# Optimization experiments

Hardware: AMD Instinct MI355X
Metric: run time of the kernel (lower is better)

## Reference

```python
import jax, jax.numpy as jnp
import numpy as np

B, S, D = 2, 2048, 1024
H, HD = 16, 64
SCALE = HD ** -0.5  # applied TWICE (q pre-scale + inference score scale), matching the source


def setup_inputs() -> dict:
    key = jax.random.key(0)
    ks = jax.random.split(key, 6)
    std = 0.02
    return {
        "x": jax.random.normal(ks[0], (B, S, D), dtype=jnp.float32),
        "Wq": jax.random.normal(ks[1], (D, D), dtype=jnp.float32) * std,
        "Wk": jax.random.normal(ks[2], (D, D), dtype=jnp.float32) * std,
        "Wv": jax.random.normal(ks[3], (D, D), dtype=jnp.float32) * std,
        "Wo": jax.random.normal(ks[4], (D, D), dtype=jnp.float32) * std,
        "bo": jnp.zeros((D,), dtype=jnp.float32),
    }


def reference(x, Wq, Wk, Wv, Wo, bo):
    b, s, d = x.shape
    # nn.Linear: y = x @ W^T ; split heads: b s (h hd) -> b h s hd
    def split_heads(y):
        return y.reshape(b, s, H, HD).transpose(0, 2, 1, 3)

    q = split_heads(x @ Wq.T) * SCALE          # forward pre-scales q
    k = split_heads(x @ Wk.T)
    v = split_heads(x @ Wv.T)

    # inference path scales scores by SCALE again (double scaling, faithful)
    scores = jnp.einsum("bhsd,bhtd->bhst", q, k) * SCALE  # [B,H,S,S]
    causal = jnp.triu(jnp.full((s, s), -jnp.inf, dtype=scores.dtype), k=1)
    scores = scores + causal[None, None]

    # explicit stable softmax as in the source
    m = jnp.max(scores, axis=-1, keepdims=True)
    e = jnp.exp(scores - m)
    attn = e / jnp.sum(e, axis=-1, keepdims=True)

    out = jnp.einsum("bhst,bhtd->bhsd", attn, v)          # [B,H,S,HD]
    out = out.transpose(0, 2, 1, 3).reshape(b, s, d)       # b h s hd -> b s (h hd)
    return out @ Wo.T + bo
```

## Files before the change

### kernel.cpp

```cpp
#include <hip/hip_runtime.h>
#include <stdint.h>

#define S_LEN 2048
#define DMODEL 1024
#define NHEAD 16
#define HDIM 64
#define BATCH 2

typedef float f32x4 __attribute__((ext_vector_type(4)));
typedef __bf16 bf16x8 __attribute__((ext_vector_type(8)));

typedef const void __attribute__((address_space(1)))* as1_cvp;
typedef void __attribute__((address_space(3)))* as3_vp;

__device__ __forceinline__ ushort f2bf(float f) {
    union { float f; unsigned u; } v; v.f = f;
    unsigned u = v.u;
    return (ushort)((u + 0x7fffu + ((u >> 16) & 1u)) >> 16);
}

__device__ __forceinline__ void gload16(const void* g, void* l) {
    __builtin_amdgcn_global_load_lds((as1_cvp)g, (as3_vp)l, 16, 0, 0);
}

template<int N> __device__ __forceinline__ void wait_vm_barrier() {
    if constexpr (N == 0)      asm volatile("s_waitcnt vmcnt(0)" ::: "memory");
    else if constexpr (N == 3) asm volatile("s_waitcnt vmcnt(3)" ::: "memory");
    else if constexpr (N == 4) asm volatile("s_waitcnt vmcnt(4)" ::: "memory");
    else                       asm volatile("s_waitcnt vmcnt(0)" ::: "memory");
    asm volatile("s_barrier" ::: "memory");
}

__global__ __launch_bounds__(256) void cvt_all(
    const float* __restrict__ x,  const float* __restrict__ wq,
    const float* __restrict__ wk, const float* __restrict__ wv,
    const float* __restrict__ wo,
    ushort* __restrict__ xb, ushort* __restrict__ wqkv, ushort* __restrict__ wob,
    float qscale) {
    const float* src; ushort* dst; int n; float sc = 1.0f;
    const int DD = DMODEL * DMODEL;
    switch (blockIdx.y) {
        case 0: src = x;  dst = xb;            n = BATCH * S_LEN * DMODEL; break;
        case 1: src = wq; dst = wqkv;          n = DD; sc = qscale; break;
        case 2: src = wk; dst = wqkv + DD;     n = DD; break;
        case 3: src = wv; dst = wqkv + 2 * DD; n = DD; break;
        default: src = wo; dst = wob;          n = DD; break;
    }
    const int step = gridDim.x * 256 * 8;
    for (int i = (blockIdx.x * 256 + threadIdx.x) * 8; i < n; i += step) {
        float4 a = *(const float4*)(src + i);
        float4 b = *(const float4*)(src + i + 4);
        union { ushort us[8]; int4 v; } r;
        r.us[0] = f2bf(a.x * sc); r.us[1] = f2bf(a.y * sc);
        r.us[2] = f2bf(a.z * sc); r.us[3] = f2bf(a.w * sc);
        r.us[4] = f2bf(b.x * sc); r.us[5] = f2bf(b.y * sc);
        r.us[6] = f2bf(b.z * sc); r.us[7] = f2bf(b.w * sc);
        *(int4*)(dst + i) = r.v;
    }
}

template<int BM, int BN, bool F32OUT, bool BIAS>
__global__ __launch_bounds__(256) void gemm_nt(
    const ushort* __restrict__ A, const ushort* __restrict__ B,
    void* __restrict__ Cv, const float* __restrict__ bias,
    int M, int N, int K) {
    __shared__ ushort As0[BM][32], As1[BM][32], As2[BM][32];
    __shared__ ushort Bs0[BN][32], Bs1[BN][32], Bs2[BN][32];
    constexpr int MR = BM / 32, NR = BN / 32, AG = BM / 64, BG = BN / 64;
    constexpr int LPS = AG + BG;
    const int tid = threadIdx.x;
    const int wave = tid >> 6, lane = tid & 63;
    const int wm = (wave >> 1) * (BM / 2), wn = (wave & 1) * (BN / 2);
    const int bm = blockIdx.x * BM, bn = blockIdx.y * BN;
    const int l15 = lane & 15, lg = lane >> 4;
    f32x4 acc[MR][NR] = {};

    const int sr = lane >> 2, scol = (lane & 3) * 8;
    const ushort* gA[AG]; const ushort* gB[BG];
    int rA0[AG], rB0[BG];
#pragma unroll
    for (int i = 0; i < AG; i++) {
        rA0[i] = wave * (BM / 4) + i * 16;
        gA[i] = A + (size_t)(bm + rA0[i] + sr) * K + scol;
    }
#pragma unroll
    for (int i = 0; i < BG; i++) {
        rB0[i] = wave * (BN / 4) + i * 16;
        gB[i] = B + (size_t)(bn + rB0[i] + sr) * K + scol;
    }

    auto STAGE = [&](int t, ushort (*as)[32], ushort (*bs)[32]) {
        const int off = t * 32;
#pragma unroll
        for (int i = 0; i < AG; i++) gload16(gA[i] + off, &as[rA0[i]][0]);
#pragma unroll
        for (int i = 0; i < BG; i++) gload16(gB[i] + off, &bs[rB0[i]][0]);
    };
    auto COMPUTE = [&](ushort (*as)[32], ushort (*bs)[32]) {
        bf16x8 af[MR], bfr[NR];
#pragma unroll
        for (int m = 0; m < MR; m++) {
            int4 t_ = *(const int4*)&as[wm + m * 16 + l15][lg * 8];
            af[m] = __builtin_bit_cast(bf16x8, t_);
        }
#pragma unroll
        for (int n = 0; n < NR; n++) {
            int4 t_ = *(const int4*)&bs[wn + n * 16 + l15][lg * 8];
            bfr[n] = __builtin_bit_cast(bf16x8, t_);
        }
        __builtin_amdgcn_s_setprio(1);
#pragma unroll
        for (int m = 0; m < MR; m++)
#pragma unroll
            for (int n = 0; n < NR; n++)
                acc[m][n] = __builtin_amdgcn_mfma_f32_16x16x32_bf16(af[m], bfr[n], acc[m][n], 0, 0, 0);
        __builtin_amdgcn_s_setprio(0);
    };

    const int NT = K / 32;
    STAGE(0, As0, Bs0);
    STAGE(1, As1, Bs1);
    wait_vm_barrier<LPS>();

    int t = 0;
    for (; t + 5 <= NT; t += 3) {
        STAGE(t + 2, As2, Bs2); COMPUTE(As0, Bs0); wait_vm_barrier<LPS>();
        STAGE(t + 3, As0, Bs0); COMPUTE(As1, Bs1); wait_vm_barrier<LPS>();
        STAGE(t + 4, As1, Bs1); COMPUTE(As2, Bs2); wait_vm_barrier<LPS>();
    }
    COMPUTE(As0, Bs0);
    wait_vm_barrier<0>();
    COMPUTE(As1, Bs1);

    float* Cf = (float*)Cv;
    ushort* Cb = (ushort*)Cv;
#pragma unroll
    for (int m = 0; m < MR; m++) {
        const int row = bm + wm + m * 16 + lg * 4;
#pragma unroll
        for (int n = 0; n < NR; n++) {
            const int col = bn + wn + n * 16 + l15;
            const float bb = BIAS ? bias[col] : 0.0f;
#pragma unroll
            for (int j = 0; j < 4; j++) {
                float v = acc[m][n][j];
                if (F32OUT) Cf[(size_t)(row + j) * N + col] = v + bb;
                else        Cb[(size_t)(row + j) * N + col] = f2bf(v);
            }
        }
    }
}

__global__ __launch_bounds__(256) void attn_fwd(
    const ushort* __restrict__ QKV, ushort* __restrict__ Og) {
    __shared__ ushort Ks[2][64][72];
    __shared__ ushort Vt[2][64][72];
    __shared__ ushort Ps[4][16][76];
    const int tid = threadIdx.x;
    const int wave = tid >> 6, lane = tid & 63;
    const int l15 = lane & 15, lg = lane >> 4;
    const int qt = 31 - (blockIdx.x >> 5);
    const int bh = blockIdx.x & 31;
    const int b = bh >> 4, h = bh & 15;
    const int q0 = qt * 64;
    const ushort* Qb = QKV + (size_t)b * S_LEN * 3072 + h * HDIM;
    const ushort* Kb = Qb + 1024;
    const ushort* Vb = Qb + 2048;

    const int4 onesi = {0x3F803F80, 0x3F803F80, 0x3F803F80, 0x3F803F80};
    const bf16x8 ones = __builtin_bit_cast(bf16x8, onesi);

    bf16x8 qf[2];
#pragma unroll
    for (int kk = 0; kk < 2; kk++) {
        int4 t = *(const int4*)(Qb + (size_t)(q0 + wave * 16 + l15) * 3072 + kk * 32 + lg * 8);
        qf[kk] = __builtin_bit_cast(bf16x8, t);
    }

    f32x4 o[4] = {};
    f32x4 lacc = {};

    const int kr = tid >> 2, kc = (tid & 3) * 8;
    const int vt_ = tid & 63, vh = (tid >> 6) * 8;
    int4 kreg0, kreg1, vreg0, vreg1;

    auto LOAD = [&](int t) {
        const ushort* kp = Kb + (size_t)(t * 64 + kr) * 3072 + kc;
        kreg0 = *(const int4*)kp;
        kreg1 = *(const int4*)(kp + 32);
        const ushort* vp = Vb + (size_t)(t * 64 + vt_) * 3072 + vh;
        vreg0 = *(const int4*)vp;
        vreg1 = *(const int4*)(vp + 32);
    };
    auto STORE = [&](int buf) {
        *(int4*)&Ks[buf][kr][kc]      = kreg0;
        *(int4*)&Ks[buf][kr][kc + 32] = kreg1;
        union { int4 v; ushort us[8]; } u0, u1;
        u0.v = vreg0; u1.v = vreg1;
#pragma unroll
        for (int j = 0; j < 8; j++) Vt[buf][vh + j][vt_] = u0.us[j];
#pragma unroll
        for (int j = 0; j < 8; j++) Vt[buf][32 + vh + j][vt_] = u1.us[j];
    };

    auto COMPUTE = [&](bool diag, int cur) {
        f32x4 s[4] = {};
        __builtin_amdgcn_s_setprio(1);
#pragma unroll
        for (int kk = 0; kk < 2; kk++) {
#pragma unroll
            for (int n = 0; n < 4; n++) {
                int4 t = *(const int4*)&Ks[cur][n * 16 + l15][kk * 32 + lg * 8];
                s[n] = __builtin_amdgcn_mfma_f32_16x16x32_bf16(qf[kk], __builtin_bit_cast(bf16x8, t), s[n], 0, 0, 0);
            }
        }
        __builtin_amdgcn_s_setprio(0);
        if (diag) {
            const int qrow = wave * 16 + lg * 4;
#pragma unroll
            for (int n = 0; n < 4; n++) {
                const int tg = n * 16 + l15;
#pragma unroll
                for (int j = 0; j < 4; j++)
                    if (tg > qrow + j) s[n][j] = -1e30f;
            }
        }
#pragma unroll
        for (int n = 0; n < 4; n++)
#pragma unroll
            for (int j = 0; j < 4; j++)
                Ps[wave][lg * 4 + j][n * 16 + l15] = f2bf(__expf(s[n][j]));
        asm volatile("s_waitcnt lgkmcnt(0)" ::: "memory");
        __builtin_amdgcn_s_setprio(1);
#pragma unroll
        for (int kk = 0; kk < 2; kk++) {
            int4 tp = *(const int4*)&Ps[wave][l15][kk * 32 + lg * 8];
            bf16x8 pf = __builtin_bit_cast(bf16x8, tp);
#pragma unroll
            for (int n = 0; n < 4; n++) {
                int4 tv = *(const int4*)&Vt[cur][n * 16 + l15][kk * 32 + lg * 8];
                o[n] = __builtin_amdgcn_mfma_f32_16x16x32_bf16(pf, __builtin_bit_cast(bf16x8, tv), o[n], 0, 0, 0);
            }
            lacc = __builtin_amdgcn_mfma_f32_16x16x32_bf16(pf, ones, lacc, 0, 0, 0);
        }
        __builtin_amdgcn_s_setprio(0);
    };

    LOAD(0);
    STORE(0);
    __syncthreads();

    for (int t0 = 0; t0 <= qt; ++t0) {
        const int cur = t0 & 1;
        if (t0 < qt) LOAD(t0 + 1);
        COMPUTE(t0 == qt, cur);
        if (t0 < qt) {
            STORE(cur ^ 1);
            __syncthreads();
        }
    }

#pragma unroll
    for (int j = 0; j < 4; j++) lacc[j] = 1.0f / lacc[j];
#pragma unroll
    for (int n = 0; n < 4; n++)
#pragma unroll
        for (int j = 0; j < 4; j++) {
            const int qrow = q0 + wave * 16 + lg * 4 + j;
            Og[((size_t)(b * S_LEN + qrow)) * DMODEL + h * HDIM + n * 16 + l15] = f2bf(o[n][j] * lacc[j]);
        }
}

extern "C" void kernel_launch(void* const* d_in, const int* in_sizes, int n_in,
                              void* d_out, int out_size, void* d_ws, size_t ws_size,
                              hipStream_t stream) {
    (void)in_sizes; (void)n_in; (void)out_size; (void)ws_size;
    const float* x  = (const float*)d_in[0];
    const float* Wq = (const float*)d_in[1];
    const float* Wk = (const float*)d_in[2];
    const float* Wv = (const float*)d_in[3];
    const float* Wo = (const float*)d_in[4];
    const float* bo = (const float*)d_in[5];
    float* out = (float*)d_out;

    const int M = BATCH * S_LEN;
    const int D = DMODEL;

    char* ws = (char*)d_ws;
    ushort* xb   = (ushort*)ws; ws += (size_t)M * D * 2;
    ushort* wqkv = (ushort*)ws; ws += (size_t)3 * D * D * 2;
    ushort* wob  = (ushort*)ws; ws += (size_t)D * D * 2;
    ushort* qkvb = (ushort*)ws; ws += (size_t)M * 3 * D * 2;
    ushort* ao   = (ushort*)ws; ws += (size_t)M * D * 2;

    const float qscale = 1.0f / 64.0f;
    cvt_all<<<dim3(512, 5), 256, 0, stream>>>(x, Wq, Wk, Wv, Wo, xb, wqkv, wob, qscale);

    gemm_nt<128, 128, false, false><<<dim3(M / 128, 3 * D / 128), 256, 0, stream>>>(
        xb, wqkv, qkvb, nullptr, M, 3 * D, D);

    attn_fwd<<<dim3(32 * BATCH * NHEAD), 256, 0, stream>>>(qkvb, ao);

    gemm_nt<64, 128, true, true><<<dim3(M / 64, D / 128), 256, 0, stream>>>(
        ao, wob, out, bo, M, D, D);
}
```

Before: 191.0 us.

## Transpose QK^T MFMA, pack P stores with cvt_pk_bf16, single-buffer K/V LDS

The A and B operands of the QK^T MFMA are swapped so each lane holds scores for consecutive key columns of one query row. P can then be written to LDS as packed 8-byte stores built with v_cvt_pk_bf16_f32, replacing scalar rounding and 2-byte stores. K/V shared memory drops from double to single buffering with padding 68, which cuts LDS use and may raise occupancy. The cost is an extra __syncthreads per tile before the store, which reduces overlap between compute and the LDS writes.

Result: no change. 189.5 us (-0.8%).

```diff
diff --git a/kernel.cpp b/kernel.cpp
--- a/kernel.cpp
+++ b/kernel.cpp
@@ -17,6 +17,12 @@
     union { float f; unsigned u; } v; v.f = f;
     unsigned u = v.u;
     return (ushort)((u + 0x7fffu + ((u >> 16) & 1u)) >> 16);
+}
+
+__device__ __forceinline__ unsigned cvt_pk_bf16(float lo, float hi) {
+    unsigned r;
+    asm("v_cvt_pk_bf16_f32 %0, %1, %2" : "=v"(r) : "v"(lo), "v"(hi));
+    return r;
 }
 
 __device__ __forceinline__ void gload16(const void* g, void* l) {
@@ -153,8 +159,8 @@
 
 __global__ __launch_bounds__(256) void attn_fwd(
     const ushort* __restrict__ QKV, ushort* __restrict__ Og) {
-    __shared__ ushort Ks[2][64][72];
-    __shared__ ushort Vt[2][64][72];
+    __shared__ ushort Ks[64][68];
+    __shared__ ushort Vt[64][68];
     __shared__ ushort Ps[4][16][76];
     const int tid = threadIdx.x;
     const int wave = tid >> 6, lane = tid & 63;
@@ -192,44 +198,45 @@
         vreg0 = *(const int4*)vp;
         vreg1 = *(const int4*)(vp + 32);
     };
-    auto STORE = [&](int buf) {
-        *(int4*)&Ks[buf][kr][kc]      = kreg0;
-        *(int4*)&Ks[buf][kr][kc + 32] = kreg1;
+    auto STORE = [&]() {
+        *(int4*)&Ks[kr][kc]      = kreg0;
+        *(int4*)&Ks[kr][kc + 32] = kreg1;
         union { int4 v; ushort us[8]; } u0, u1;
         u0.v = vreg0; u1.v = vreg1;
 #pragma unroll
-        for (int j = 0; j < 8; j++) Vt[buf][vh + j][vt_] = u0.us[j];
-#pragma unroll
-        for (int j = 0; j < 8; j++) Vt[buf][32 + vh + j][vt_] = u1.us[j];
-    };
-
-    auto COMPUTE = [&](bool diag, int cur) {
+        for (int j = 0; j < 8; j++) Vt[vh + j][vt_] = u0.us[j];
+#pragma unroll
+        for (int j = 0; j < 8; j++) Vt[32 + vh + j][vt_] = u1.us[j];
+    };
+
+    auto COMPUTE = [&](bool diag) {
         f32x4 s[4] = {};
         __builtin_amdgcn_s_setprio(1);
 #pragma unroll
         for (int kk = 0; kk < 2; kk++) {
 #pragma unroll
             for (int n = 0; n < 4; n++) {
-                int4 t = *(const int4*)&Ks[cur][n * 16 + l15][kk * 32 + lg * 8];
-                s[n] = __builtin_amdgcn_mfma_f32_16x16x32_bf16(qf[kk], __builtin_bit_cast(bf16x8, t), s[n], 0, 0, 0);
+                int4 t = *(const int4*)&Ks[n * 16 + l15][kk * 32 + lg * 8];
+                s[n] = __builtin_amdgcn_mfma_f32_16x16x32_bf16(__builtin_bit_cast(bf16x8, t), qf[kk], s[n], 0, 0, 0);
             }
         }
         __builtin_amdgcn_s_setprio(0);
         if (diag) {
-            const int qrow = wave * 16 + lg * 4;
+            const int ql = wave * 16 + l15;
 #pragma unroll
             for (int n = 0; n < 4; n++) {
-                const int tg = n * 16 + l15;
 #pragma unroll
                 for (int j = 0; j < 4; j++)
-                    if (tg > qrow + j) s[n][j] = -1e30f;
+                    if (n * 16 + lg * 4 + j > ql) s[n][j] = -1e30f;
             }
         }
 #pragma unroll
-        for (int n = 0; n < 4; n++)
-#pragma unroll
-            for (int j = 0; j < 4; j++)
-                Ps[wave][lg * 4 + j][n * 16 + l15] = f2bf(__expf(s[n][j]));
+        for (int n = 0; n < 4; n++) {
+            unsigned lo = cvt_pk_bf16(__expf(s[n][0]), __expf(s[n][1]));
+            unsigned hi = cvt_pk_bf16(__expf(s[n][2]), __expf(s[n][3]));
+            uint2 w; w.x = lo; w.y = hi;
+            *(uint2*)&Ps[wave][l15][n * 16 + lg * 4] = w;
+        }
         asm volatile("s_waitcnt lgkmcnt(0)" ::: "memory");
         __builtin_amdgcn_s_setprio(1);
 #pragma unroll
@@ -238,7 +245,7 @@
             bf16x8 pf = __builtin_bit_cast(bf16x8, tp);
 #pragma unroll
             for (int n = 0; n < 4; n++) {
-                int4 tv = *(const int4*)&Vt[cur][n * 16 + l15][kk * 32 + lg * 8];
+                int4 tv = *(const int4*)&Vt[n * 16 + l15][kk * 32 + lg * 8];
                 o[n] = __builtin_amdgcn_mfma_f32_16x16x32_bf16(pf, __builtin_bit_cast(bf16x8, tv), o[n], 0, 0, 0);
             }
             lacc = __builtin_amdgcn_mfma_f32_16x16x32_bf16(pf, ones, lacc, 0, 0, 0);
@@ -247,15 +254,15 @@
     };
 
     LOAD(0);
-    STORE(0);
+    STORE();
     __syncthreads();
 
     for (int t0 = 0; t0 <= qt; ++t0) {
-        const int cur = t0 & 1;
         if (t0 < qt) LOAD(t0 + 1);
-        COMPUTE(t0 == qt, cur);
+        COMPUTE(t0 == qt);
         if (t0 < qt) {
-            STORE(cur ^ 1);
+            __syncthreads();
+            STORE();
             __syncthreads();
         }
     }
```
